# Optimization experiments

Measured on AMD Instinct MI355X. Metric: run time of the kernel, lower is better.

The kernel has to match this reference:

```python
import jax, jax.numpy as jnp
import numpy as np

K = 3  # spline order
G = 5  # grid_size

def bspline(x):
    # Cox-de Boor B-spline basis over uniform grid on [-1,1] extended by K knots each side.
    h = 2.0 / G
    grid = jnp.arange(-K, G + K + 1, dtype=x.dtype) * h - 1.0  # [G+2K+1]
    xe = x[..., None]
    b = ((xe >= grid[:-1]) & (xe < grid[1:])).astype(x.dtype)  # order-0 bases [..., G+2K]
    for p in range(1, K + 1):
        b = ((xe - grid[:-(p + 1)]) / (grid[p:-1] - grid[:-(p + 1)]) * b[..., :-1]
             + (grid[p + 1:] - xe) / (grid[p + 1:] - grid[1:-p]) * b[..., 1:])
    return b  # [..., G+K]

def kan_conv(x, wb, ws, k):
    # x: [B,Cin,H,W] -> patches [B, Cin*k*k, H', W'] -> KANLinear per spatial position
    p = jax.lax.conv_general_dilated_patches(x, (k, k), (1, 1), 'VALID')
    p = jnp.moveaxis(p, 1, -1)  # [B,H',W',F]
    base = jax.nn.silu(p) @ wb.T
    spline = jnp.einsum('bhwig,oig->bhwo', bspline(p), ws)
    return jnp.moveaxis(base + spline, -1, 1)  # [B,Cout,H',W']

def maxpool2(x):
    return jax.lax.reduce_window(x, -jnp.inf, jax.lax.max, (1, 1, 2, 2), (1, 1, 2, 2), 'VALID')

def setup_inputs() -> dict:
    key = jax.random.key(0)
    ks = jax.random.split(key, 9)
    B = 4096
    s = 0.1
    return {
        'x': jax.random.normal(ks[0], (B, 1, 28, 28), jnp.float32),
        'wb1': jax.random.normal(ks[1], (5, 9), jnp.float32) * s,
        'ws1': jax.random.normal(ks[2], (5, 9, G + K), jnp.float32) * s,
        'wb2': jax.random.normal(ks[3], (5, 125), jnp.float32) * s,
        'ws2': jax.random.normal(ks[4], (5, 125, G + K), jnp.float32) * s,
        'wb3': jax.random.normal(ks[5], (2, 45), jnp.float32) * s,
        'ws3': jax.random.normal(ks[6], (2, 45, G + K), jnp.float32) * s,
        'fc_w': jax.random.normal(ks[7], (200, 98), jnp.float32) * s,
        'fc_b': jnp.zeros((200,), jnp.float32),
    }

def reference(x, wb1, ws1, wb2, ws2, wb3, ws3, fc_w, fc_b):
    h = kan_conv(x, wb1, ws1, 3)    # [B,5,26,26]
    h = maxpool2(h)                 # [B,5,13,13]
    h = kan_conv(h, wb2, ws2, 5)    # [B,5,9,9]
    h = kan_conv(h, wb3, ws3, 3)    # [B,2,7,7]
    h = h.reshape(h.shape[0], -1)   # [B,98]
    return h @ fc_w.T + fc_b        # [B,200]
```

## Files before the change

kernel.cpp:

```cpp
#include <hip/hip_runtime.h>


typedef _Float16 h2 __attribute__((ext_vector_type(2)));
typedef _Float16 f16x8 __attribute__((ext_vector_type(8)));
typedef float f32x4 __attribute__((ext_vector_type(4)));
typedef unsigned int uint_t;
typedef unsigned long long u64;

__device__ __forceinline__ h2 as_h2(uint_t u) { union { uint_t u; h2 h; } c; c.u = u; return c.h; }
__device__ __forceinline__ uint_t pk(float a, float b) {
    h2 v; v[0] = (_Float16)a; v[1] = (_Float16)b;
    union { h2 h; uint_t u; } c; c.h = v; return c.u;
}

__device__ __forceinline__ float silu_f(float v) {
    return v / (1.0f + __expf(-v));
}

struct RecW { u64 R0, R1; uint_t R2; };
__device__ __forceinline__ RecW rec_words(float v) {
    float s  = silu_f(v);
    float t  = (v + 2.2f) * 2.5f;
    float cf = floorf(t);
    int   c  = (int)cf;
    float u  = t - cf;
    float u2 = u * u, u3 = u2 * u;
    float w  = 1.0f - u;
    const float k6 = 0.16666667f;
    float n0 = k6 * u3;
    float n1 = k6 * (-3.0f * u3 + 3.0f * u2 + 3.0f * u + 1.0f);
    float n2 = k6 * (3.0f * u3 - 6.0f * u2 + 4.0f);
    float n3 = k6 * (w * w * w);
    u64 H = ((u64)pk(n1, n0) << 32) | (u64)pk(n3, n2);
    if ((unsigned)c > 10u) H = 0;
    int cc = c < 0 ? 0 : (c > 10 ? 10 : c);
    int L  = cc * 16 - 48;
    u64 sl_lo = (L < 64) ? (H << (L & 63)) : 0;
    u64 hi_a  = (L == 0) ? 0 : (H >> ((64 - L) & 63));
    u64 hi_b  = H << ((L - 64) & 63);
    u64 sl_hi = (L < 64) ? hi_a : hi_b;
    u64 sr    = H >> ((-L) & 63);
    u64 B0 = (L >= 0) ? sl_lo : sr;
    u64 B1 = (L >= 0) ? sl_hi : 0;
    RecW r;
    r.R0 = (B0 << 16) | (u64)pk(s, 0.0f);
    r.R1 = (B0 >> 48) | (B1 << 16);
    r.R2 = (uint_t)(B1 >> 48);
    return r;
}

__device__ __forceinline__ void write_rec16s(_Float16* p, int off, float v) {
    RecW rw = rec_words(v);
    uint4 lo, hi;
    lo.x = (uint_t)rw.R0; lo.y = (uint_t)(rw.R0 >> 32);
    lo.z = (uint_t)rw.R1; lo.w = (uint_t)(rw.R1 >> 32);
    hi.x = rw.R2; hi.y = 0; hi.z = 0; hi.w = 0;
    *(uint4*)(p + off)       = lo;
    *(uint4*)(p + (8 ^ off)) = hi;
}

__device__ __forceinline__ void write_rec10(_Float16* p, float v) {
    RecW rw = rec_words(v);
    uint_t* d = (uint_t*)p;
    d[0] = (uint_t)rw.R0; d[1] = (uint_t)(rw.R0 >> 32);
    d[2] = (uint_t)rw.R1; d[3] = (uint_t)(rw.R1 >> 32);
    d[4] = rw.R2;
}

#define FCWT_BYTE_OFF   0
#define W1COL_BYTE_OFF  78400
#define W2COL_BYTE_OFF  80320
#define W3COL_BYTE_OFF  99520

__global__ __launch_bounds__(256) void kan_prep(
    const float* __restrict__ wb1, const float* __restrict__ ws1,
    const float* __restrict__ wb2, const float* __restrict__ ws2,
    const float* __restrict__ wb3, const float* __restrict__ ws3,
    const float* __restrict__ fcw, float* __restrict__ fcwT,
    _Float16* __restrict__ w1col, _Float16* __restrict__ w2col,
    _Float16* __restrict__ w3col)
{
    int gtid = blockIdx.x * 256 + threadIdx.x;
    int gstr = gridDim.x * 256;
    for (int i = gtid; i < 19600; i += gstr) {
        int o = i / 98, j = i % 98;
        fcwT[j * 200 + o] = fcw[i];
    }
    for (int i = gtid; i < 960; i += gstr) {
        int n = i / 160, k = i % 160;
        int rec = k >> 4, f = k & 15;
        float v = 0.f;
        if (n < 5 && rec < 9 && f < 9)
            v = (f == 0) ? wb1[n * 9 + rec] : ws1[(n * 9 + rec) * 8 + (f - 1)];
        w1col[i] = (_Float16)v;
    }
    for (int i = gtid; i < 9600; i += gstr) {
        int n = i / 1600, k2 = i % 1600;
        int tap = k2 >> 6, k = k2 & 63;
        int di = tap / 5, dj = tap % 5;
        int c = k / 10, f = k % 10;
        float v = 0.f;
        if (n < 5 && k < 50 && f < 9) {
            int r = n * 125 + c * 25 + di * 5 + dj;
            v = (f == 0) ? wb2[r] : ws2[r * 8 + (f - 1)];
        }
        w2col[i] = (_Float16)v;
    }
    for (int i = gtid; i < 3456; i += gstr) {
        int n = i / 576, k2 = i % 576;
        int tap = k2 >> 6, k = k2 & 63;
        int di = tap / 3, dj = tap % 3;
        int c = k / 10, f = k % 10;
        float v = 0.f;
        if (n < 2 && k < 50 && f < 9) {
            int r = n * 45 + c * 9 + di * 3 + dj;
            v = (f == 0) ? wb3[r] : ws3[r * 8 + (f - 1)];
        }
        w3col[i] = (_Float16)v;
    }
}

__global__ __launch_bounds__(256) void kan_fused(
    const float* __restrict__ x,
    const _Float16* __restrict__ w1col,
    const _Float16* __restrict__ w2col,
    const _Float16* __restrict__ w3col,
    const float* __restrict__ fcwT,
    const float* __restrict__ fcb,
    float* __restrict__ out)
{
    __shared__ __align__(16) _Float16 smemA[12544];
    __shared__ __align__(16) float    smemB[1696];
    _Float16* P2h   = (_Float16*)smemB;
    float*    part2 = smemB;
    float*    h3f   = smemB;

    const int b   = blockIdx.x;
    const int tid = threadIdx.x;
    const int wv  = __builtin_amdgcn_readfirstlane(tid >> 6);
    const int ln  = tid & 63;

    const int m   = ln & 15;
    const int kb  = ln >> 4;
    const int hr  = kb >> 1;
    const int s8  = (kb & 1) * 8;
    const int nn  = m < 5 ? m : 5;

#pragma unroll 1
    for (int i = tid; i < 784; i += 256)
        write_rec16s(&smemA[i * 16], (i & 4) << 1, x[b * 784 + i]);
    __syncthreads();

    {
        f16x8 Bf[5];
#pragma unroll
        for (int ks = 0; ks < 5; ++ks)
            Bf[ks] = *(const f16x8*)(w1col + nn * 160 + ks * 32 + kb * 8);
        const int dpix[10] = {0, 1, 2, 28, 29, 30, 56, 57, 58, 0};
#pragma unroll 1
        for (int tile = wv; tile < 43; tile += 4) {
            int p = tile * 16 + m; p = p > 675 ? 675 : p;
            int pix0 = (p / 26) * 28 + (p % 26);
            f32x4 acc = {0.f, 0.f, 0.f, 0.f};
#pragma unroll
            for (int ks = 0; ks < 5; ++ks) {
                int dp = hr ? dpix[2 * ks + 1] : dpix[2 * ks];
                int p2 = pix0 + dp;
                int addr = p2 * 16 + (s8 ^ ((p2 & 4) << 1));
                f16x8 av = *(const f16x8*)(smemA + addr);
                acc = __builtin_amdgcn_mfma_f32_16x16x32_f16(av, Bf[ks], acc, 0, 0, 0);
            }
            int srow = tile * 16 + kb * 4;
#pragma unroll
            for (int r = 0; r < 4; ++r) {
                int s = srow + r;
                if (m < 5 && s < 676) P2h[m * 676 + s] = (_Float16)acc[r];
            }
        }
    }
    __syncthreads();

#pragma unroll 1
    for (int i = tid; i < 845; i += 256) {
        int c = i / 169, pp = i % 169;
        int ph = pp / 13, pw = pp % 13;
        const _Float16* q = P2h + c * 676 + (2 * ph) * 26 + 2 * pw;
        h2 a = as_h2(*(const uint_t*)q);
        h2 d = as_h2(*(const uint_t*)(q + 26));
        float mx = fmaxf(fmaxf((float)a[0], (float)a[1]),
                         fmaxf((float)d[0], (float)d[1]));
        write_rec10(&smemA[pp * 72 + c * 10], mx);
    }
    __syncthreads();

    {
        int ryb[6];
#pragma unroll
        for (int t = 0; t < 6; ++t) {
            int p = t * 16 + m; p = p > 80 ? 80 : p;
            ryb[t] = (p / 9) * 13 + (p % 9);
        }
        f32x4 acc[6];
#pragma unroll
        for (int t = 0; t < 6; ++t) { f32x4 z = {0.f,0.f,0.f,0.f}; acc[t] = z; }
#pragma unroll 1
        for (int tap = wv; tap < 25; tap += 4) {
            int di = tap / 5, dj = tap % 5;
            const _Float16* wrow = w2col + nn * 1600 + tap * 64 + kb * 8;
            f16x8 bv0 = *(const f16x8*)(wrow);
            f16x8 bv1 = *(const f16x8*)(wrow + 32);
            int qoff = di * 13 + dj;
#pragma unroll
            for (int t = 0; t < 6; ++t) {
                const _Float16* ab = smemA + (ryb[t] + qoff) * 72 + kb * 8;
                acc[t] = __builtin_amdgcn_mfma_f32_16x16x32_f16(
                             *(const f16x8*)(ab), bv0, acc[t], 0, 0, 0);
                acc[t] = __builtin_amdgcn_mfma_f32_16x16x32_f16(
                             *(const f16x8*)(ab + 32), bv1, acc[t], 0, 0, 0);
            }
        }
        int prow = kb * 4;
#pragma unroll
        for (int t = 0; t < 6; ++t) {
#pragma unroll
            for (int r = 0; r < 4; ++r) {
                int pp = t * 16 + prow + r;
                if (m < 5 && pp < 81) part2[(wv * 5 + m) * 81 + pp] = acc[t][r];
            }
        }
    }
    __syncthreads();

#pragma unroll 1
    for (int i = tid; i < 405; i += 256) {
        int o = i / 81, pp = i % 81;
        float v = part2[(0 * 5 + o) * 81 + pp] + part2[(1 * 5 + o) * 81 + pp]
                + part2[(2 * 5 + o) * 81 + pp] + part2[(3 * 5 + o) * 81 + pp];
        write_rec10(&smemA[pp * 72 + o * 10], v);
    }
    __syncthreads();

    {
        int p3 = wv * 16 + m; p3 = p3 > 48 ? 48 : p3;
        int ry3 = (p3 / 7) * 9 + (p3 % 7);
        f32x4 acc = {0.f, 0.f, 0.f, 0.f};
#pragma unroll 1
        for (int tap = 0; tap < 9; ++tap) {
            int di = tap / 3, dj = tap % 3;
            const _Float16* wrow = w3col + nn * 576 + tap * 64 + kb * 8;
            f16x8 bv0 = *(const f16x8*)(wrow);
            f16x8 bv1 = *(const f16x8*)(wrow + 32);
            const _Float16* ab = smemA + (ry3 + di * 9 + dj) * 72 + kb * 8;
            acc = __builtin_amdgcn_mfma_f32_16x16x32_f16(*(const f16x8*)(ab),      bv0, acc, 0, 0, 0);
            acc = __builtin_amdgcn_mfma_f32_16x16x32_f16(*(const f16x8*)(ab + 32), bv1, acc, 0, 0, 0);
        }
#pragma unroll
        for (int r = 0; r < 4; ++r) {
            int pout = wv * 16 + kb * 4 + r;
            if (m < 2 && pout < 49) h3f[m * 49 + pout] = acc[r];
        }
    }
    __syncthreads();

    if (tid < 200) {
        float a0 = 0.f, a1 = 0.f;
#pragma unroll 7
        for (int j = 0; j < 98; j += 2) {
            a0 += fcwT[j * 200 + tid]       * h3f[j];
            a1 += fcwT[(j + 1) * 200 + tid] * h3f[j + 1];
        }
        out[b * 200 + tid] = fcb[tid] + a0 + a1;
    }
}

extern "C" void kernel_launch(void* const* d_in, const int* in_sizes, int n_in,
                              void* d_out, int out_size, void* d_ws, size_t ws_size,
                              hipStream_t stream) {
    const float* x   = (const float*)d_in[0];
    const float* wb1 = (const float*)d_in[1];
    const float* ws1 = (const float*)d_in[2];
    const float* wb2 = (const float*)d_in[3];
    const float* ws2 = (const float*)d_in[4];
    const float* wb3 = (const float*)d_in[5];
    const float* ws3 = (const float*)d_in[6];
    const float* fcw = (const float*)d_in[7];
    const float* fcb = (const float*)d_in[8];
    float* out = (float*)d_out;

    float*    fcwT  = (float*)((char*)d_ws + FCWT_BYTE_OFF);
    _Float16* w1col = (_Float16*)((char*)d_ws + W1COL_BYTE_OFF);
    _Float16* w2col = (_Float16*)((char*)d_ws + W2COL_BYTE_OFF);
    _Float16* w3col = (_Float16*)((char*)d_ws + W3COL_BYTE_OFF);

    kan_prep<<<32, 256, 0, stream>>>(wb1, ws1, wb2, ws2, wb3, ws3, fcw,
                                     fcwT, w1col, w2col, w3col);

    int B = in_sizes[0] / 784;
    kan_fused<<<B, 256, 0, stream>>>(x, w1col, w2col, w3col, fcwT, fcb, out);
}
```

Baseline: 146.1 us.

## Fold column taps into MFMA N dimension for conv2/conv3, shift-add outputs

Conv2 and conv3 now put the (output channel, column offset dj) pairs into the MFMA N dimension. Each wave computes full-width rows over the padded 13- or 9-wide input grid, and a shift-and-add pass over an fp16 staging buffer in shared memory assembles the outputs. This cuts the number of MFMA issues and drops the cross-wave partial-sum reduction that the tap-split approach needed. The FC weights are also stored as fp16 to halve their load traffic. The fp16 intermediates and fp16 FC weights reduce precision, and the padded rows add some wasted compute.

```diff
diff --git a/kernel.cpp b/kernel.cpp
--- a/kernel.cpp
+++ b/kernel.cpp
@@ -67,24 +67,24 @@
     d[4] = rw.R2;
 }
 
-#define FCWT_BYTE_OFF   0
-#define W1COL_BYTE_OFF  78400
-#define W2COL_BYTE_OFF  80320
-#define W3COL_BYTE_OFF  99520
+#define FCWT16_BYTE_OFF 0
+#define W1COL_BYTE_OFF  39200
+#define W2N_BYTE_OFF    41120
+#define W3N_BYTE_OFF    61600
 
 __global__ __launch_bounds__(256) void kan_prep(
     const float* __restrict__ wb1, const float* __restrict__ ws1,
     const float* __restrict__ wb2, const float* __restrict__ ws2,
     const float* __restrict__ wb3, const float* __restrict__ ws3,
-    const float* __restrict__ fcw, float* __restrict__ fcwT,
-    _Float16* __restrict__ w1col, _Float16* __restrict__ w2col,
-    _Float16* __restrict__ w3col)
+    const float* __restrict__ fcw, _Float16* __restrict__ fcwT16,
+    _Float16* __restrict__ w1col, _Float16* __restrict__ w2n,
+    _Float16* __restrict__ w3n)
 {
     int gtid = blockIdx.x * 256 + threadIdx.x;
     int gstr = gridDim.x * 256;
     for (int i = gtid; i < 19600; i += gstr) {
         int o = i / 98, j = i % 98;
-        fcwT[j * 200 + o] = fcw[i];
+        fcwT16[j * 200 + o] = (_Float16)fcw[i];
     }
     for (int i = gtid; i < 960; i += gstr) {
         int n = i / 160, k = i % 160;
@@ -94,46 +94,48 @@
             v = (f == 0) ? wb1[n * 9 + rec] : ws1[(n * 9 + rec) * 8 + (f - 1)];
         w1col[i] = (_Float16)v;
     }
-    for (int i = gtid; i < 9600; i += gstr) {
-        int n = i / 1600, k2 = i % 1600;
-        int tap = k2 >> 6, k = k2 & 63;
-        int di = tap / 5, dj = tap % 5;
-        int c = k / 10, f = k % 10;
+    for (int i = gtid; i < 10240; i += gstr) {
+        int pass = i / 5120, rem = i % 5120;
+        int n = rem / 320, k = rem % 320;
+        int di = k / 64, q = k % 64;
+        int c = q / 10, f = q % 10;
         float v = 0.f;
-        if (n < 5 && k < 50 && f < 9) {
-            int r = n * 125 + c * 25 + di * 5 + dj;
+        bool nvalid = pass == 0 ? (n < 15) : (n < 10);
+        if (nvalid && q < 50 && f < 9) {
+            int o  = pass == 0 ? n / 3 : n / 2;
+            int dj = pass == 0 ? n % 3 : 3 + n % 2;
+            int r = o * 125 + c * 25 + di * 5 + dj;
             v = (f == 0) ? wb2[r] : ws2[r * 8 + (f - 1)];
         }
-        w2col[i] = (_Float16)v;
-    }
-    for (int i = gtid; i < 3456; i += gstr) {
-        int n = i / 576, k2 = i % 576;
-        int tap = k2 >> 6, k = k2 & 63;
-        int di = tap / 3, dj = tap % 3;
-        int c = k / 10, f = k % 10;
+        w2n[i] = (_Float16)v;
+    }
+    for (int i = gtid; i < 3072; i += gstr) {
+        int n = i / 192, k = i % 192;
+        int di = k / 64, q = k % 64;
+        int c = q / 10, f = q % 10;
         float v = 0.f;
-        if (n < 2 && k < 50 && f < 9) {
-            int r = n * 45 + c * 9 + di * 3 + dj;
+        if (n < 6 && q < 50 && f < 9) {
+            int o = n / 3, dj = n % 3;
+            int r = o * 45 + c * 9 + di * 3 + dj;
             v = (f == 0) ? wb3[r] : ws3[r * 8 + (f - 1)];
         }
-        w3col[i] = (_Float16)v;
+        w3n[i] = (_Float16)v;
     }
 }
 
 __global__ __launch_bounds__(256) void kan_fused(
     const float* __restrict__ x,
     const _Float16* __restrict__ w1col,
-    const _Float16* __restrict__ w2col,
-    const _Float16* __restrict__ w3col,
-    const float* __restrict__ fcwT,
+    const _Float16* __restrict__ w2n,
+    const _Float16* __restrict__ w3n,
+    const _Float16* __restrict__ fcwT16,
     const float* __restrict__ fcb,
     float* __restrict__ out)
 {
     __shared__ __align__(16) _Float16 smemA[12544];
     __shared__ __align__(16) float    smemB[1696];
-    _Float16* P2h   = (_Float16*)smemB;
-    float*    part2 = smemB;
-    float*    h3f   = smemB;
+    _Float16* P2h = (_Float16*)smemB;
+    float*    h3f = smemB;
 
     const int b   = blockIdx.x;
     const int tid = threadIdx.x;
@@ -194,71 +196,86 @@
     __syncthreads();
 
     {
-        int ryb[6];
-#pragma unroll
-        for (int t = 0; t < 6; ++t) {
-            int p = t * 16 + m; p = p > 80 ? 80 : p;
-            ryb[t] = (p / 9) * 13 + (p % 9);
-        }
-        f32x4 acc[6];
-#pragma unroll
-        for (int t = 0; t < 6; ++t) { f32x4 z = {0.f,0.f,0.f,0.f}; acc[t] = z; }
-#pragma unroll 1
-        for (int tap = wv; tap < 25; tap += 4) {
-            int di = tap / 5, dj = tap % 5;
-            const _Float16* wrow = w2col + nn * 1600 + tap * 64 + kb * 8;
-            f16x8 bv0 = *(const f16x8*)(wrow);
-            f16x8 bv1 = *(const f16x8*)(wrow + 32);
-            int qoff = di * 13 + dj;
-#pragma unroll
-            for (int t = 0; t < 6; ++t) {
-                const _Float16* ab = smemA + (ryb[t] + qoff) * 72 + kb * 8;
-                acc[t] = __builtin_amdgcn_mfma_f32_16x16x32_f16(
-                             *(const f16x8*)(ab), bv0, acc[t], 0, 0, 0);
-                acc[t] = __builtin_amdgcn_mfma_f32_16x16x32_f16(
-                             *(const f16x8*)(ab + 32), bv1, acc[t], 0, 0, 0);
-            }
-        }
-        int prow = kb * 4;
-#pragma unroll
-        for (int t = 0; t < 6; ++t) {
-#pragma unroll
-            for (int r = 0; r < 4; ++r) {
-                int pp = t * 16 + prow + r;
-                if (m < 5 && pp < 81) part2[(wv * 5 + m) * 81 + pp] = acc[t][r];
-            }
-        }
-    }
-    __syncthreads();
-
-#pragma unroll 1
-    for (int i = tid; i < 405; i += 256) {
-        int o = i / 81, pp = i % 81;
-        float v = part2[(0 * 5 + o) * 81 + pp] + part2[(1 * 5 + o) * 81 + pp]
-                + part2[(2 * 5 + o) * 81 + pp] + part2[(3 * 5 + o) * 81 + pp];
-        write_rec10(&smemA[pp * 72 + o * 10], v);
+        int p0 = wv * 16 + m;
+        int p1 = (wv + 4) * 16 + m;
+        f32x4 a00 = {0.f,0.f,0.f,0.f}, a01 = {0.f,0.f,0.f,0.f};
+        f32x4 a10 = {0.f,0.f,0.f,0.f}, a11 = {0.f,0.f,0.f,0.f};
+#pragma unroll 1
+        for (int s = 0; s < 10; ++s) {
+            int di  = s >> 1;
+            int off = (s & 1) * 32;
+            f16x8 bv0 = *(const f16x8*)(w2n + m * 320 + s * 32 + kb * 8);
+            f16x8 bv1 = *(const f16x8*)(w2n + 5120 + m * 320 + s * 32 + kb * 8);
+            int rp0 = p0 + di * 13; rp0 = rp0 > 168 ? 168 : rp0;
+            int rp1 = p1 + di * 13; rp1 = rp1 > 168 ? 168 : rp1;
+            f16x8 av0 = *(const f16x8*)(smemA + rp0 * 72 + off + kb * 8);
+            f16x8 av1 = *(const f16x8*)(smemA + rp1 * 72 + off + kb * 8);
+            a00 = __builtin_amdgcn_mfma_f32_16x16x32_f16(av0, bv0, a00, 0, 0, 0);
+            a01 = __builtin_amdgcn_mfma_f32_16x16x32_f16(av0, bv1, a01, 0, 0, 0);
+            a10 = __builtin_amdgcn_mfma_f32_16x16x32_f16(av1, bv0, a10, 0, 0, 0);
+            a11 = __builtin_amdgcn_mfma_f32_16x16x32_f16(av1, bv1, a11, 0, 0, 0);
+        }
+        __syncthreads();
+        _Float16* C2 = smemA + 8192;
+#pragma unroll
+        for (int r = 0; r < 4; ++r) {
+            int r0 = wv * 16 + kb * 4 + r;
+            int r1 = (wv + 4) * 16 + kb * 4 + r;
+            C2[r0 * 32 + m]      = (_Float16)a00[r];
+            C2[r0 * 32 + 16 + m] = (_Float16)a01[r];
+            C2[r1 * 32 + m]      = (_Float16)a10[r];
+            C2[r1 * 32 + 16 + m] = (_Float16)a11[r];
+        }
     }
     __syncthreads();
 
     {
-        int p3 = wv * 16 + m; p3 = p3 > 48 ? 48 : p3;
-        int ry3 = (p3 / 7) * 9 + (p3 % 7);
+        const _Float16* C2 = smemA + 8192;
+#pragma unroll 1
+        for (int i = tid; i < 405; i += 256) {
+            int o = i / 81, pp = i % 81;
+            int y = pp / 9, xx = pp % 9;
+            int base = (y * 13 + xx) * 32;
+            float v = (float)C2[base +        o * 3]
+                    + (float)C2[base +  32 +  o * 3 + 1]
+                    + (float)C2[base +  64 +  o * 3 + 2]
+                    + (float)C2[base +  96 + 16 + o * 2]
+                    + (float)C2[base + 128 + 16 + o * 2 + 1];
+            write_rec10(&smemA[pp * 72 + o * 10], v);
+        }
+    }
+    __syncthreads();
+
+    {
+        int p3 = wv * 16 + m;
         f32x4 acc = {0.f, 0.f, 0.f, 0.f};
-#pragma unroll 1
-        for (int tap = 0; tap < 9; ++tap) {
-            int di = tap / 3, dj = tap % 3;
-            const _Float16* wrow = w3col + nn * 576 + tap * 64 + kb * 8;
-            f16x8 bv0 = *(const f16x8*)(wrow);
-            f16x8 bv1 = *(const f16x8*)(wrow + 32);
-            const _Float16* ab = smemA + (ry3 + di * 9 + dj) * 72 + kb * 8;
-            acc = __builtin_amdgcn_mfma_f32_16x16x32_f16(*(const f16x8*)(ab),      bv0, acc, 0, 0, 0);
-            acc = __builtin_amdgcn_mfma_f32_16x16x32_f16(*(const f16x8*)(ab + 32), bv1, acc, 0, 0, 0);
-        }
+#pragma unroll
+        for (int s = 0; s < 6; ++s) {
+            int di  = s >> 1;
+            int off = (s & 1) * 32;
+            f16x8 bv = *(const f16x8*)(w3n + m * 192 + s * 32 + kb * 8);
+            int rp = p3 + di * 9; rp = rp > 80 ? 80 : rp;
+            f16x8 av = *(const f16x8*)(smemA + rp * 72 + off + kb * 8);
+            acc = __builtin_amdgcn_mfma_f32_16x16x32_f16(av, bv, acc, 0, 0, 0);
+        }
+        _Float16* C3 = smemA + 8192;
 #pragma unroll
         for (int r = 0; r < 4; ++r) {
-            int pout = wv * 16 + kb * 4 + r;
-            if (m < 2 && pout < 49) h3f[m * 49 + pout] = acc[r];
-        }
+            int row = wv * 16 + kb * 4 + r;
+            C3[row * 16 + m] = (_Float16)acc[r];
+        }
+    }
+    __syncthreads();
+
+    if (tid < 98) {
+        const _Float16* C3 = smemA + 8192;
+        int o = tid / 49, pout = tid % 49;
+        int y = pout / 7, xx = pout % 7;
+        int base = (y * 9 + xx) * 16;
+        float v = (float)C3[base +      o * 3]
+                + (float)C3[base + 16 + o * 3 + 1]
+                + (float)C3[base + 32 + o * 3 + 2];
+        h3f[tid] = v;
     }
     __syncthreads();
 
@@ -266,8 +283,8 @@
         float a0 = 0.f, a1 = 0.f;
 #pragma unroll 7
         for (int j = 0; j < 98; j += 2) {
-            a0 += fcwT[j * 200 + tid]       * h3f[j];
-            a1 += fcwT[(j + 1) * 200 + tid] * h3f[j + 1];
+            a0 += (float)fcwT16[j * 200 + tid]       * h3f[j];
+            a1 += (float)fcwT16[(j + 1) * 200 + tid] * h3f[j + 1];
         }
         out[b * 200 + tid] = fcb[tid] + a0 + a1;
     }
@@ -287,14 +304,14 @@
     const float* fcb = (const float*)d_in[8];
     float* out = (float*)d_out;
 
-    float*    fcwT  = (float*)((char*)d_ws + FCWT_BYTE_OFF);
-    _Float16* w1col = (_Float16*)((char*)d_ws + W1COL_BYTE_OFF);
-    _Float16* w2col = (_Float16*)((char*)d_ws + W2COL_BYTE_OFF);
-    _Float16* w3col = (_Float16*)((char*)d_ws + W3COL_BYTE_OFF);
+    _Float16* fcwT16 = (_Float16*)((char*)d_ws + FCWT16_BYTE_OFF);
+    _Float16* w1col  = (_Float16*)((char*)d_ws + W1COL_BYTE_OFF);
+    _Float16* w2n    = (_Float16*)((char*)d_ws + W2N_BYTE_OFF);
+    _Float16* w3n    = (_Float16*)((char*)d_ws + W3N_BYTE_OFF);
 
     kan_prep<<<32, 256, 0, stream>>>(wb1, ws1, wb2, ws2, wb3, ws3, fcw,
-                                     fcwT, w1col, w2col, w3col);
+                                     fcwT16, w1col, w2n, w3n);
 
     int B = in_sizes[0] / 784;
-    kan_fused<<<B, 256, 0, stream>>>(x, w1col, w2col, w3col, fcwT, fcb, out);
-}
+    kan_fused<<<B, 256, 0, stream>>>(x, w1col, w2n, w3n, fcwT16, fcb, out);
+}
```

Result: slower. 158.6 us (+8.5%).
